# Performance work log

Hardware: AMD Instinct MI355X
Metric: run time of the kernel (lower is better)

Reference implementation:

```python
import jax, jax.numpy as jnp
import numpy as np

B, S, J, D = 8, 512, 25, 64      # batch, seq_len, n_joints, d_model
H, DH = 8, 32                    # n_heads, d_head
IN, OUT = J * D, J * DH * H      # 1600, 6400


def setup_inputs() -> dict:
    key = jax.random.key(0)
    ks = jax.random.split(key, 5)
    sc_in = 1.0 / np.sqrt(IN)
    sc_hd = 1.0 / np.sqrt(DH * H)
    return {
        "x": jax.random.normal(ks[0], (B, S, J, D), dtype=jnp.float32),
        # weights stored [in, out] (transpose of torch Linear.weight)
        "Wq": jax.random.normal(ks[1], (IN, OUT), dtype=jnp.float32) * sc_in,
        "Wk": jax.random.normal(ks[2], (IN, OUT), dtype=jnp.float32) * sc_in,
        "Wv": jax.random.normal(ks[3], (IN, OUT), dtype=jnp.float32) * sc_in,
        "Wb": jax.random.normal(ks[4], (DH * H, D), dtype=jnp.float32) * sc_hd,
    }


def reference(x, Wq, Wk, Wv, Wb):
    b, s, j, d = x.shape
    xf = x.reshape(b, s, j * d)                      # [B,S,J*D]
    q = xf @ Wq                                      # [B,S,OUT]
    k = xf @ Wk
    v = xf @ Wv
    # single fused attention over the full J*d_head*H width, scaled by d_model
    scores = jnp.einsum("bse,bte->bst", q, k) * (d ** -0.5)  # [B,S,S]
    causal = jnp.triu(jnp.ones((s, s), dtype=bool), k=1)
    scores = jnp.where(causal[None], -jnp.inf, scores)
    attn = jax.nn.softmax(scores, axis=-1)           # [B,S,S]
    ctx = jnp.einsum("bst,bte->bse", attn, v)        # [B,S,OUT]
    ctx = ctx.reshape(b, s, j, DH * H)               # [B,S,J,dh*H]
    out = ctx @ Wb                                   # [B,S,J,D]  (dropout = eval identity)
    return out
```

## Files before the change

### kernel.cpp

```cpp
#include <hip/hip_runtime.h>

typedef float  f32x4  __attribute__((ext_vector_type(4)));
typedef __bf16 bf16x8 __attribute__((ext_vector_type(8)));
typedef __bf16 bf16x4 __attribute__((ext_vector_type(4)));

__device__ __forceinline__ void gl_lds16(const void* g, void* l) {
    __builtin_amdgcn_global_load_lds(
        (const __attribute__((address_space(1))) void*)g,
        (__attribute__((address_space(3))) void*)l, 16, 0, 0);
}

__device__ __forceinline__ int xcd_swz(int wg, int nwg) {
    int xcd = wg & 7, idx = wg >> 3;
    int q = nwg >> 3, r = nwg & 7;
    return (xcd < r ? xcd * (q + 1) : r * (q + 1) + (xcd - r) * q) + idx;
}

__global__ void split_f32(const float* __restrict__ in, __bf16* __restrict__ hi,
                          __bf16* __restrict__ lo, long n) {
    long i = ((long)blockIdx.x * blockDim.x + threadIdx.x) * 4;
    if (i >= n) return;
    float4 v = *(const float4*)&in[i];
    bf16x4 h, l;
    h[0] = (__bf16)v.x; l[0] = (__bf16)(v.x - (float)h[0]);
    h[1] = (__bf16)v.y; l[1] = (__bf16)(v.y - (float)h[1]);
    h[2] = (__bf16)v.z; l[2] = (__bf16)(v.z - (float)h[2]);
    h[3] = (__bf16)v.w; l[3] = (__bf16)(v.w - (float)h[3]);
    *(bf16x4*)&hi[i] = h;
    *(bf16x4*)&lo[i] = l;
}

__global__ void split2_f32(const float* __restrict__ a, const float* __restrict__ b,
                           __bf16* __restrict__ ah, __bf16* __restrict__ al,
                           __bf16* __restrict__ bh, __bf16* __restrict__ bl, long n) {
    long i = ((long)blockIdx.x * blockDim.x + threadIdx.x) * 4;
    const float* src = a;
    __bf16 *dh = ah, *dl = al;
    if (i >= n) { i -= n; src = b; dh = bh; dl = bl; }
    if (i >= n) return;
    float4 v = *(const float4*)&src[i];
    bf16x4 h, l;
    h[0] = (__bf16)v.x; l[0] = (__bf16)(v.x - (float)h[0]);
    h[1] = (__bf16)v.y; l[1] = (__bf16)(v.y - (float)h[1]);
    h[2] = (__bf16)v.z; l[2] = (__bf16)(v.z - (float)h[2]);
    h[3] = (__bf16)v.w; l[3] = (__bf16)(v.w - (float)h[3]);
    *(bf16x4*)&dh[i] = h;
    *(bf16x4*)&dl[i] = l;
}

__global__ void copy_f32(const float* __restrict__ in, float* __restrict__ out) {
    long i = ((long)blockIdx.x * blockDim.x + threadIdx.x) * 4;
    *(float4*)&out[i] = *(const float4*)&in[i];
}

__global__ void cvt_wb(const float* __restrict__ Wb, __bf16* __restrict__ Wbt) {
    int idx = blockIdx.x * 256 + threadIdx.x;
    int k = idx >> 6, n = idx & 63;
    Wbt[n * 256 + k] = (__bf16)Wb[idx];
}

__global__ __launch_bounds__(256) void wvb_kernel(const float* __restrict__ Wv,
                                                  const __bf16* __restrict__ Wbt,
                                                  __bf16* __restrict__ WvbT) {
    const int kb = blockIdx.x;
    const int j  = blockIdx.y;
    const int tid = threadIdx.x;
    const int w = tid >> 6, l = tid & 63;
    const long r0 = (long)kb * 64 + w * 16;
    const int lr = l & 15, lk8 = (l >> 4) * 8;
    f32x4 acc[4];
    #pragma unroll
    for (int n = 0; n < 4; ++n) acc[n] = (f32x4){0.f, 0.f, 0.f, 0.f};
    #pragma unroll
    for (int kt = 0; kt < 8; ++kt) {
        const int k = kt * 32 + lk8;
        const float* ap = &Wv[(r0 + lr) * 6400 + j * 256 + k];
        float4 f0 = *(const float4*)ap;
        float4 f1 = *(const float4*)(ap + 4);
        bf16x8 a = {(__bf16)f0.x, (__bf16)f0.y, (__bf16)f0.z, (__bf16)f0.w,
                    (__bf16)f1.x, (__bf16)f1.y, (__bf16)f1.z, (__bf16)f1.w};
        #pragma unroll
        for (int n = 0; n < 4; ++n) {
            bf16x8 b = *(const bf16x8*)&Wbt[(n * 16 + lr) * 256 + k];
            acc[n] = __builtin_amdgcn_mfma_f32_16x16x32_bf16(a, b, acc[n], 0, 0, 0);
        }
    }
    const int rr = (l >> 4) * 4;
    #pragma unroll
    for (int n = 0; n < 4; ++n)
        #pragma unroll
        for (int r = 0; r < 4; ++r)
            WvbT[(long)(j * 64 + n * 16 + lr) * 1600 + r0 + rr + r] = (__bf16)acc[n][r];
}

template <int OUTMODE, bool CAUSAL, bool SWZ>
__global__ __launch_bounds__(256) void gemm3f(
    const __bf16* __restrict__ Ahi, const __bf16* __restrict__ Alo,
    const __bf16* __restrict__ Bhi, const __bf16* __restrict__ Blo,
    float* __restrict__ C, __bf16* __restrict__ Ch, __bf16* __restrict__ Cl,
    int ktot, int nkc, int lda, int ldb, int ldc, int M, int N,
    long sA, long sB, long sC, float scale)
{
    __shared__ __bf16 AsH[8192], AsL[8192], BsH[8192], BsL[8192];
    int bx = blockIdx.x, by = blockIdx.y;
    if (SWZ) {
        int f = xcd_swz(by * gridDim.x + bx, gridDim.x * gridDim.y);
        bx = f % gridDim.x; by = f / gridDim.x;
    }
    const int n0 = bx * 128, m0 = by * 128;
    if (CAUSAL && n0 > m0) return;
    const int bz = blockIdx.z;
    const int batch = bz / nkc, kc = bz % nkc;
    Ahi += (long)batch * sA; Alo += (long)batch * sA;
    Bhi += (long)batch * sB; Blo += (long)batch * sB;
    const int kbeg = (kc * ktot) / nkc;
    const int kend = ((kc + 1) * ktot) / nkc;

    const int tid = threadIdx.x;
    const int w = tid >> 6, l = tid & 63;
    const int wr = w >> 1, wc = w & 1;
    const int lr = l & 15;
    const int lk8 = (l >> 4) * 8;
    const int kswz = (lr & 7) << 3;
    const int srow = l >> 3;
    const int scol = ((l & 7) ^ (l >> 3)) * 8;

    f32x4 acc[4][4];
    #pragma unroll
    for (int m = 0; m < 4; ++m)
        #pragma unroll
        for (int n = 0; n < 4; ++n) acc[m][n] = (f32x4){0.f, 0.f, 0.f, 0.f};

    for (int kt = kbeg; kt < kend; ++kt) {
        const int k0 = kt << 6;
        __syncthreads();
        #pragma unroll
        for (int it = 0; it < 4; ++it) {
            const int j = it * 4 + w;
            const int grow = j * 8 + srow;
            const long ga = (long)(m0 + grow) * lda + k0 + scol;
            const long gb = (long)(n0 + grow) * ldb + k0 + scol;
            gl_lds16(Ahi + ga, &AsH[j * 512]);
            gl_lds16(Alo + ga, &AsL[j * 512]);
            gl_lds16(Bhi + gb, &BsH[j * 512]);
            gl_lds16(Blo + gb, &BsL[j * 512]);
        }
        __syncthreads();
        #pragma unroll
        for (int kk = 0; kk < 2; ++kk) {
            const int kx = (kk * 32 + lk8) ^ kswz;
            bf16x8 ah[4], bh[4], tt[4];
            #pragma unroll
            for (int m = 0; m < 4; ++m)
                ah[m] = *(const bf16x8*)&AsH[(wr * 64 + m * 16 + lr) * 64 + kx];
            #pragma unroll
            for (int n = 0; n < 4; ++n)
                bh[n] = *(const bf16x8*)&BsH[(wc * 64 + n * 16 + lr) * 64 + kx];
            #pragma unroll
            for (int m = 0; m < 4; ++m)
                #pragma unroll
                for (int n = 0; n < 4; ++n)
                    acc[m][n] = __builtin_amdgcn_mfma_f32_16x16x32_bf16(ah[m], bh[n], acc[m][n], 0, 0, 0);
            #pragma unroll
            for (int n = 0; n < 4; ++n)
                tt[n] = *(const bf16x8*)&BsL[(wc * 64 + n * 16 + lr) * 64 + kx];
            #pragma unroll
            for (int m = 0; m < 4; ++m)
                #pragma unroll
                for (int n = 0; n < 4; ++n)
                    acc[m][n] = __builtin_amdgcn_mfma_f32_16x16x32_bf16(ah[m], tt[n], acc[m][n], 0, 0, 0);
            #pragma unroll
            for (int m = 0; m < 4; ++m)
                tt[m] = *(const bf16x8*)&AsL[(wr * 64 + m * 16 + lr) * 64 + kx];
            #pragma unroll
            for (int m = 0; m < 4; ++m)
                #pragma unroll
                for (int n = 0; n < 4; ++n)
                    acc[m][n] = __builtin_amdgcn_mfma_f32_16x16x32_bf16(tt[m], bh[n], acc[m][n], 0, 0, 0);
        }
    }

    const int r0 = wr * 64 + (l >> 4) * 4;
    const int c0 = wc * 64 + lr;
    #pragma unroll
    for (int m = 0; m < 4; ++m)
        #pragma unroll
        for (int n = 0; n < 4; ++n)
            #pragma unroll
            for (int r = 0; r < 4; ++r) {
                int row = m0 + r0 + m * 16 + r;
                int col = n0 + c0 + n * 16;
                if (row < M && col < N) {
                    float v = acc[m][n][r] * scale;
                    long idx = (long)batch * sC + (long)row * ldc + col;
                    if (OUTMODE == 1) {
                        unsafeAtomicAdd(&C[idx], v);
                    } else if (OUTMODE == 2) {
                        __bf16 h = (__bf16)v;
                        Ch[idx] = h;
                        Cl[idx] = (__bf16)(v - (float)h);
                    } else {
                        C[idx] = v;
                    }
                }
            }
}

template <bool SWZ>
__global__ __launch_bounds__(256) void gemm3m(
    const __bf16* __restrict__ Ahi, const __bf16* __restrict__ Alo,
    const __bf16* __restrict__ B1h, const __bf16* __restrict__ B1l,
    const __bf16* __restrict__ B2,
    __bf16* __restrict__ Ch, __bf16* __restrict__ Cl,
    __bf16* __restrict__ Cv)
{
    __shared__ __bf16 AsH[8192], AsL[8192], BsH[8192], BsL[8192];
    int bx = blockIdx.x, by = blockIdx.y;
    if (SWZ) {
        int f = xcd_swz(by * gridDim.x + bx, gridDim.x * gridDim.y);
        bx = f % gridDim.x; by = f / gridDim.x;
    }
    const int n0 = bx * 128, m0 = by * 128;
    const int tid = threadIdx.x;
    const int w = tid >> 6, l = tid & 63;
    const int wr = w >> 1, wc = w & 1;
    const int lr = l & 15;
    const int lk8 = (l >> 4) * 8;
    const int kswz = (lr & 7) << 3;
    const int srow = l >> 3;
    const int scol = ((l & 7) ^ (l >> 3)) * 8;

    f32x4 acc[4][4];
    #pragma unroll
    for (int m = 0; m < 4; ++m)
        #pragma unroll
        for (int n = 0; n < 4; ++n) acc[m][n] = (f32x4){0.f, 0.f, 0.f, 0.f};

    if (blockIdx.z == 0) {
        for (int kt = 0; kt < 25; ++kt) {
            const int k0 = kt << 6;
            __syncthreads();
            #pragma unroll
            for (int it = 0; it < 4; ++it) {
                const int j = it * 4 + w;
                const int grow = j * 8 + srow;
                const long ga = (long)(m0 + grow) * 1600 + k0 + scol;
                const long gb = (long)(n0 + grow) * 1600 + k0 + scol;
                gl_lds16(Ahi + ga, &AsH[j * 512]);
                gl_lds16(Alo + ga, &AsL[j * 512]);
                gl_lds16(B1h + gb, &BsH[j * 512]);
                gl_lds16(B1l + gb, &BsL[j * 512]);
            }
            __syncthreads();
            #pragma unroll
            for (int kk = 0; kk < 2; ++kk) {
                const int kx = (kk * 32 + lk8) ^ kswz;
                bf16x8 ah[4], bh[4], tt[4];
                #pragma unroll
                for (int m = 0; m < 4; ++m)
                    ah[m] = *(const bf16x8*)&AsH[(wr * 64 + m * 16 + lr) * 64 + kx];
                #pragma unroll
                for (int n = 0; n < 4; ++n)
                    bh[n] = *(const bf16x8*)&BsH[(wc * 64 + n * 16 + lr) * 64 + kx];
                #pragma unroll
                for (int m = 0; m < 4; ++m)
                    #pragma unroll
                    for (int n = 0; n < 4; ++n)
                        acc[m][n] = __builtin_amdgcn_mfma_f32_16x16x32_bf16(ah[m], bh[n], acc[m][n], 0, 0, 0);
                #pragma unroll
                for (int n = 0; n < 4; ++n)
                    tt[n] = *(const bf16x8*)&BsL[(wc * 64 + n * 16 + lr) * 64 + kx];
                #pragma unroll
                for (int m = 0; m < 4; ++m)
                    #pragma unroll
                    for (int n = 0; n < 4; ++n)
                        acc[m][n] = __builtin_amdgcn_mfma_f32_16x16x32_bf16(ah[m], tt[n], acc[m][n], 0, 0, 0);
                #pragma unroll
                for (int m = 0; m < 4; ++m)
                    tt[m] = *(const bf16x8*)&AsL[(wr * 64 + m * 16 + lr) * 64 + kx];
                #pragma unroll
                for (int m = 0; m < 4; ++m)
                    #pragma unroll
                    for (int n = 0; n < 4; ++n)
                        acc[m][n] = __builtin_amdgcn_mfma_f32_16x16x32_bf16(tt[m], bh[n], acc[m][n], 0, 0, 0);
            }
        }
        const int r0 = wr * 64 + (l >> 4) * 4;
        const int c0 = wc * 64 + lr;
        #pragma unroll
        for (int m = 0; m < 4; ++m)
            #pragma unroll
            for (int n = 0; n < 4; ++n)
                #pragma unroll
                for (int r = 0; r < 4; ++r) {
                    int row = m0 + r0 + m * 16 + r;
                    int col = n0 + c0 + n * 16;
                    if (col < 1600) {
                        float v = acc[m][n][r];
                        long idx = (long)row * 1600 + col;
                        __bf16 h = (__bf16)v;
                        Ch[idx] = h;
                        Cl[idx] = (__bf16)(v - (float)h);
                    }
                }
    } else {
        for (int kt = 0; kt < 25; ++kt) {
            const int k0 = kt << 6;
            __syncthreads();
            #pragma unroll
            for (int it = 0; it < 4; ++it) {
                const int j = it * 4 + w;
                const int grow = j * 8 + srow;
                gl_lds16(Ahi + (long)(m0 + grow) * 1600 + k0 + scol, &AsH[j * 512]);
                gl_lds16(B2  + (long)(n0 + grow) * 1600 + k0 + scol, &BsH[j * 512]);
            }
            __syncthreads();
            #pragma unroll
            for (int kk = 0; kk < 2; ++kk) {
                const int kx = (kk * 32 + lk8) ^ kswz;
                bf16x8 a[4], b[4];
                #pragma unroll
                for (int m = 0; m < 4; ++m)
                    a[m] = *(const bf16x8*)&AsH[(wr * 64 + m * 16 + lr) * 64 + kx];
                #pragma unroll
                for (int n = 0; n < 4; ++n)
                    b[n] = *(const bf16x8*)&BsH[(wc * 64 + n * 16 + lr) * 64 + kx];
                #pragma unroll
                for (int m = 0; m < 4; ++m)
                    #pragma unroll
                    for (int n = 0; n < 4; ++n)
                        acc[m][n] = __builtin_amdgcn_mfma_f32_16x16x32_bf16(a[m], b[n], acc[m][n], 0, 0, 0);
            }
        }
        const int r0 = m0 + wr * 64 + (l >> 4) * 4;
        const int c0 = n0 + wc * 64 + lr;
        #pragma unroll
        for (int m = 0; m < 4; ++m)
            #pragma unroll
            for (int n = 0; n < 4; ++n)
                #pragma unroll
                for (int r = 0; r < 4; ++r) {
                    int row = r0 + m * 16 + r;
                    int col = c0 + n * 16;
                    Cv[(long)(row >> 9) * 851968 + (long)col * 512 + (row & 511)] =
                        (__bf16)acc[m][n][r];
                }
    }
}

template <typename CT, bool TRANSC, bool SWZ>
__global__ __launch_bounds__(256) void gemm_bt(const __bf16* __restrict__ A,
                                               const __bf16* __restrict__ Bt,
                                               CT* __restrict__ C,
                                               int K, int lda, int ldb, int ldc,
                                               long sA, long sB, long sC,
                                               float scale, int causal, int Nlim) {
    __shared__ __bf16 As[8192];
    __shared__ __bf16 Bs[8192];
    int bx = blockIdx.x, by = blockIdx.y;
    if (SWZ) {
        int f = xcd_swz(by * gridDim.x + bx, gridDim.x * gridDim.y);
        bx = f % gridDim.x; by = f / gridDim.x;
    }
    if (causal == 2) by = gridDim.y - 1 - by;
    const int n0 = bx * 128, m0 = by * 128;
    A  += (long)blockIdx.z * sA;
    Bt += (long)blockIdx.z * sB;
    int ksteps = K >> 6;
    if (causal == 2) { int lim = (m0 >> 6) + 2; if (lim < ksteps) ksteps = lim; }

    const int tid = threadIdx.x;
    const int w = tid >> 6, l = tid & 63;
    const int wr = w >> 1, wc = w & 1;
    const int lr = l & 15;
    const int lk8 = (l >> 4) * 8;
    const int kswz = (lr & 7) << 3;
    const int srow = l >> 3;
    const int scol = ((l & 7) ^ (l >> 3)) * 8;

    f32x4 acc[4][4];
    #pragma unroll
    for (int m = 0; m < 4; ++m)
        #pragma unroll
        for (int n = 0; n < 4; ++n) acc[m][n] = (f32x4){0.f, 0.f, 0.f, 0.f};

    for (int kt = 0; kt < ksteps; ++kt) {
        const int k0 = kt << 6;
        __syncthreads();
        #pragma unroll
        for (int it = 0; it < 4; ++it) {
            const int j = it * 4 + w;
            const int grow = j * 8 + srow;
            gl_lds16(A  + (long)(m0 + grow) * lda + k0 + scol, &As[j * 512]);
            gl_lds16(Bt + (long)(n0 + grow) * ldb + k0 + scol, &Bs[j * 512]);
        }
        __syncthreads();
        #pragma unroll
        for (int kk = 0; kk < 2; ++kk) {
            const int kx = (kk * 32 + lk8) ^ kswz;
            bf16x8 a[4], b[4];
            #pragma unroll
            for (int m = 0; m < 4; ++m)
                a[m] = *(const bf16x8*)&As[(wr * 64 + m * 16 + lr) * 64 + kx];
            #pragma unroll
            for (int n = 0; n < 4; ++n)
                b[n] = *(const bf16x8*)&Bs[(wc * 64 + n * 16 + lr) * 64 + kx];
            #pragma unroll
            for (int m = 0; m < 4; ++m)
                #pragma unroll
                for (int n = 0; n < 4; ++n)
                    acc[m][n] = __builtin_amdgcn_mfma_f32_16x16x32_bf16(a[m], b[n], acc[m][n], 0, 0, 0);
        }
    }

    const int r0 = m0 + wr * 64 + (l >> 4) * 4;
    const int c0 = n0 + wc * 64 + lr;
    #pragma unroll
    for (int m = 0; m < 4; ++m)
        #pragma unroll
        for (int n = 0; n < 4; ++n)
            #pragma unroll
            for (int r = 0; r < 4; ++r) {
                float v = acc[m][n][r] * scale;
                int row = r0 + m * 16 + r;
                int col = c0 + n * 16;
                if (TRANSC) {
                    C[(long)(row >> 9) * sC + (long)col * ldc + (row & 511)] = (CT)v;
                } else if (col < Nlim) {
                    C[(long)blockIdx.z * sC + (long)row * ldc + col] = (CT)v;
                }
            }
}

__global__ __launch_bounds__(256) void softmax_causal(const float* __restrict__ S,
                                                      __bf16* __restrict__ P) {
    __shared__ float red[8];
    const long rid = blockIdx.x;
    const int s = (int)(rid & 511);
    const float* row = S + rid * 512;
    __bf16* prow = P + rid * 512;
    const int t = threadIdx.x;
    float x0 = (t       <= s) ? row[t]       : -3.0e38f;
    float x1 = (t + 256 <= s) ? row[t + 256] : -3.0e38f;
    float m = fmaxf(x0, x1);
    #pragma unroll
    for (int off = 1; off < 64; off <<= 1) m = fmaxf(m, __shfl_xor(m, off));
    const int w = t >> 6;
    if ((t & 63) == 0) red[w] = m;
    __syncthreads();
    m = fmaxf(fmaxf(red[0], red[1]), fmaxf(red[2], red[3]));
    float e0 = __expf(x0 - m), e1 = __expf(x1 - m);
    float sum = e0 + e1;
    #pragma unroll
    for (int off = 1; off < 64; off <<= 1) sum += __shfl_xor(sum, off);
    if ((t & 63) == 0) red[4 + w] = sum;
    __syncthreads();
    sum = red[4] + red[5] + red[6] + red[7];
    const float rinv = 1.0f / sum;
    prow[t]       = (__bf16)(e0 * rinv);
    prow[t + 256] = (__bf16)(e1 * rinv);
}

extern "C" void kernel_launch(void* const* d_in, const int* in_sizes, int n_in,
                              void* d_out, int out_size, void* d_ws, size_t ws_size,
                              hipStream_t stream) {
    (void)in_sizes; (void)n_in; (void)out_size; (void)ws_size;
    const float* x  = (const float*)d_in[0];
    const float* Wq = (const float*)d_in[1];
    const float* Wk = (const float*)d_in[2];
    const float* Wv = (const float*)d_in[3];
    const float* Wb = (const float*)d_in[4];
    float* out = (float*)d_out;
    char* ws = (char*)d_ws;

    __bf16* Wqh = (__bf16*)(ws + 0);
    __bf16* Wql = (__bf16*)(ws + 20480000);
    __bf16* Wkh = (__bf16*)(ws + 40960000);
    __bf16* Wkl = (__bf16*)(ws + 61440000);
    float*  Gt  = (float*) (ws + 81920000);
    __bf16* Gth = (__bf16*)(ws + 92160000);
    __bf16* Gtl = (__bf16*)(ws + 97484800);
    __bf16* Wbt = (__bf16*)(ws + 102809600);
    __bf16* xh   = (__bf16*)(ws + 0);
    __bf16* xl   = (__bf16*)(ws + 13107200);
    __bf16* th   = (__bf16*)(ws + 26214400);
    __bf16* tl   = (__bf16*)(ws + 39321600);
    __bf16* VWt  = (__bf16*)(ws + 52428800);
    __bf16* WvbT = (__bf16*)(ws + 66060288);
    float*  s    = (float*) (ws + 81920000);
    __bf16* P    = (__bf16*)(ws + 90308608);
    float*  CtxF = (float*) (ws + 0);

    split2_f32<<<20000, 256, 0, stream>>>(Wq, Wk, Wqh, Wql, Wkh, Wkl, 10240000L);
    hipMemsetAsync(Gt, 0, 10240000, stream);
    gemm3f<1, false, true><<<dim3(13, 13, 3), 256, 0, stream>>>(
        Wkh, Wkl, Wqh, Wql, Gt, nullptr, nullptr,
        100, 3, 6400, 6400, 1600, 1600, 1600, 0L, 0L, 0L, 1.0f);
    hipMemsetAsync((char*)Gth + 5120000, 0, 204800, stream);
    hipMemsetAsync((char*)Gtl + 5120000, 0, 204800, stream);
    split_f32<<<2500, 256, 0, stream>>>(Gt, Gth, Gtl, 2560000L);

    split_f32<<<6400, 256, 0, stream>>>(x, xh, xl, 6553600L);
    cvt_wb<<<64, 256, 0, stream>>>(Wb, Wbt);
    hipMemsetAsync((char*)WvbT + 5120000, 0, 204800, stream);
    wvb_kernel<<<dim3(25, 25), 256, 0, stream>>>(Wv, Wbt, WvbT);

    gemm3m<true><<<dim3(13, 32, 2), 256, 0, stream>>>(
        xh, xl, Gth, Gtl, WvbT, th, tl, VWt);

    hipMemsetAsync(s, 0, 8388608, stream);
    gemm3f<1, true, false><<<dim3(4, 4, 40), 256, 0, stream>>>(
        th, tl, xh, xl, s, nullptr, nullptr,
        25, 5, 1600, 1600, 512, 512, 512, 819200L, 819200L, 262144L, 0.125f);

    softmax_causal<<<4096, 256, 0, stream>>>(s, P);

    gemm_bt<float, false, false><<<dim3(13, 4, 8), 256, 0, stream>>>(
        P, VWt, CtxF, 512, 512, 512, 1600,
        262144L, 851968L, 819200L, 1.0f, 2, 1600);

    copy_f32<<<6400, 256, 0, stream>>>(CtxF, out);
}
```

Before: 345.5 us.

## Use 256x256-tile split-K GEMM for the Wk·Wq Gram product

Adds a new 512-thread kernel that computes each 256x256 output tile, with 128 KB of LDS holding the hi and lo bf16 operand splits. It replaces the 128x128 kernel for the Wk^T·Wq product and changes the split-K factor from 3 to 5, giving a 7x7x5 grid of 245 blocks. The goal is more operand reuse per LDS load and a single wave of blocks across the CUs. In exchange, more padded work is done past the 1600 edge, occupancy is one block per CU with no double buffering, and more atomic adds go into the output.

New measurement: 373.9 us. +8.2%, slower.

```diff
diff --git a/kernel.cpp b/kernel.cpp
--- a/kernel.cpp
+++ b/kernel.cpp
@@ -91,6 +91,107 @@
         #pragma unroll
         for (int r = 0; r < 4; ++r)
             WvbT[(long)(j * 64 + n * 16 + lr) * 1600 + r0 + rr + r] = (__bf16)acc[n][r];
+}
+
+template <bool SWZ>
+__global__ __launch_bounds__(512, 2) void gemm3w(
+    const __bf16* __restrict__ Ahi, const __bf16* __restrict__ Alo,
+    const __bf16* __restrict__ Bhi, const __bf16* __restrict__ Blo,
+    float* __restrict__ C,
+    int ktot, int nkc, int lda, int ldb, int ldc, int M, int N, float scale)
+{
+    __shared__ __bf16 AsH[16384], AsL[16384], BsH[16384], BsL[16384];
+    int bx = blockIdx.x, by = blockIdx.y;
+    if (SWZ) {
+        int f = xcd_swz(by * gridDim.x + bx, gridDim.x * gridDim.y);
+        bx = f % gridDim.x; by = f / gridDim.x;
+    }
+    const int n0 = bx * 256, m0 = by * 256;
+    const int kc = blockIdx.z;
+    const int kbeg = (kc * ktot) / nkc;
+    const int kend = ((kc + 1) * ktot) / nkc;
+
+    const int tid = threadIdx.x;
+    const int w = tid >> 6, l = tid & 63;
+    const int wm = w >> 2, wn = w & 3;
+    const int lr = l & 15;
+    const int lk8 = (l >> 4) * 8;
+    const int kswz = (lr & 7) << 3;
+    const int srow = l >> 3;
+    const int scol = ((l & 7) ^ (l >> 3)) * 8;
+
+    f32x4 acc[8][4];
+    #pragma unroll
+    for (int mf = 0; mf < 8; ++mf)
+        #pragma unroll
+        for (int nf = 0; nf < 4; ++nf) acc[mf][nf] = (f32x4){0.f, 0.f, 0.f, 0.f};
+
+    for (int kt = kbeg; kt < kend; ++kt) {
+        const int k0 = kt << 6;
+        __syncthreads();
+        #pragma unroll
+        for (int it = 0; it < 4; ++it) {
+            const int j = it * 8 + w;
+            const int grow = j * 8 + srow;
+            const long ga = (long)(m0 + grow) * lda + k0 + scol;
+            const long gb = (long)(n0 + grow) * ldb + k0 + scol;
+            gl_lds16(Ahi + ga, &AsH[j * 512]);
+            gl_lds16(Alo + ga, &AsL[j * 512]);
+            gl_lds16(Bhi + gb, &BsH[j * 512]);
+            gl_lds16(Blo + gb, &BsL[j * 512]);
+        }
+        __syncthreads();
+        #pragma unroll
+        for (int kk = 0; kk < 2; ++kk) {
+            const int kx = (kk * 32 + lk8) ^ kswz;
+            bf16x8 ah[8], bh[4];
+            #pragma unroll
+            for (int mf = 0; mf < 8; ++mf)
+                ah[mf] = *(const bf16x8*)&AsH[(wm * 128 + mf * 16 + lr) * 64 + kx];
+            #pragma unroll
+            for (int nf = 0; nf < 4; ++nf)
+                bh[nf] = *(const bf16x8*)&BsH[(wn * 64 + nf * 16 + lr) * 64 + kx];
+            #pragma unroll
+            for (int mf = 0; mf < 8; ++mf)
+                #pragma unroll
+                for (int nf = 0; nf < 4; ++nf)
+                    acc[mf][nf] = __builtin_amdgcn_mfma_f32_16x16x32_bf16(ah[mf], bh[nf], acc[mf][nf], 0, 0, 0);
+            {
+                bf16x8 bl[4];
+                #pragma unroll
+                for (int nf = 0; nf < 4; ++nf)
+                    bl[nf] = *(const bf16x8*)&BsL[(wn * 64 + nf * 16 + lr) * 64 + kx];
+                #pragma unroll
+                for (int mf = 0; mf < 8; ++mf)
+                    #pragma unroll
+                    for (int nf = 0; nf < 4; ++nf)
+                        acc[mf][nf] = __builtin_amdgcn_mfma_f32_16x16x32_bf16(ah[mf], bl[nf], acc[mf][nf], 0, 0, 0);
+            }
+            {
+                #pragma unroll
+                for (int mf = 0; mf < 8; ++mf) {
+                    bf16x8 al = *(const bf16x8*)&AsL[(wm * 128 + mf * 16 + lr) * 64 + kx];
+                    #pragma unroll
+                    for (int nf = 0; nf < 4; ++nf)
+                        acc[mf][nf] = __builtin_amdgcn_mfma_f32_16x16x32_bf16(al, bh[nf], acc[mf][nf], 0, 0, 0);
+                }
+            }
+        }
+    }
+
+    const int rbase = m0 + wm * 128 + (l >> 4) * 4;
+    const int cbase = n0 + wn * 64 + lr;
+    #pragma unroll
+    for (int mf = 0; mf < 8; ++mf)
+        #pragma unroll
+        for (int nf = 0; nf < 4; ++nf)
+            #pragma unroll
+            for (int r = 0; r < 4; ++r) {
+                int row = rbase + mf * 16 + r;
+                int col = cbase + nf * 16;
+                if (row < M && col < N)
+                    unsafeAtomicAdd(&C[(long)row * ldc + col], acc[mf][nf][r] * scale);
+            }
 }
 
 template <int OUTMODE, bool CAUSAL, bool SWZ>
@@ -493,9 +594,9 @@
 
     split2_f32<<<20000, 256, 0, stream>>>(Wq, Wk, Wqh, Wql, Wkh, Wkl, 10240000L);
     hipMemsetAsync(Gt, 0, 10240000, stream);
-    gemm3f<1, false, true><<<dim3(13, 13, 3), 256, 0, stream>>>(
-        Wkh, Wkl, Wqh, Wql, Gt, nullptr, nullptr,
-        100, 3, 6400, 6400, 1600, 1600, 1600, 0L, 0L, 0L, 1.0f);
+    gemm3w<true><<<dim3(7, 7, 5), 512, 0, stream>>>(
+        Wkh, Wkl, Wqh, Wql, Gt,
+        100, 5, 6400, 6400, 1600, 1600, 1600, 1.0f);
     hipMemsetAsync((char*)Gth + 5120000, 0, 204800, stream);
     hipMemsetAsync((char*)Gtl + 5120000, 0, 204800, stream);
     split_f32<<<2500, 256, 0, stream>>>(Gt, Gth, Gtl, 2560000L);
```
